# Kernel optimization log

Measured on AMD Instinct MI355X. Metric: run time of the kernel, lower is better.

Reference implementation:

```python
import jax, jax.numpy as jnp
import numpy as np

N, E, D = 50000, 800000, 128
BN_EPS = 1e-5


def mish(x):
    return x * jnp.tanh(jax.nn.softplus(x))


def setup_inputs() -> dict:
    key = jax.random.key(0)
    ks = jax.random.split(key, 16)
    s = 1.0 / np.sqrt(D)
    s2 = 1.0 / np.sqrt(2 * D)
    # unique (row, col) edge pairs so the dense-adjacency edge norm reduces
    # exactly to conv_w[bond_type] + conv_b per edge
    rng = np.random.default_rng(0)
    codes = np.unique(rng.integers(0, N * N, size=2 * E, dtype=np.int64))[:E]
    edge_index = jnp.asarray(np.stack([codes // N, codes % N]), dtype=jnp.int32)
    bond_types = jnp.asarray(rng.integers(0, 4, size=E), dtype=jnp.int32)

    def nrm(k, shape, sc):
        return jax.random.normal(k, shape, jnp.float32) * sc

    return {
        "x": nrm(ks[0], (N, D), 1.0),
        "coords": nrm(ks[1], (N, 3), 1.0),
        "edge_index": edge_index,
        "bond_types": bond_types,
        # NodeFeaturePath
        "W_nb": nrm(ks[2], (2 * D, D), s2), "b_nb": jnp.zeros((D,), jnp.float32),
        "W_nout": nrm(ks[3], (D, D), s), "b_nout": jnp.zeros((D,), jnp.float32),
        # EdgeFeaturePath (1x1 conv over 4 bond-type channels -> scalar per edge)
        "conv_w": nrm(ks[4], (4,), 0.5), "conv_b": jnp.zeros((), jnp.float32),
        "W_el": nrm(ks[5], (2 * D, D), s2), "b_el": jnp.zeros((D,), jnp.float32),
        "W_eout": nrm(ks[6], (D, D), s), "b_eout": jnp.zeros((D,), jnp.float32),
        # StructuralFeaturePath
        "W_coord": nrm(ks[7], (2 * D, D), s2), "b_coord": jnp.zeros((D,), jnp.float32),
        "W_pair": nrm(ks[8], (D, D), s), "b_pair": jnp.zeros((D,), jnp.float32),
        "W_sout": nrm(ks[9], (2 * D, D), s2), "b_sout": jnp.zeros((D,), jnp.float32),
        # FeatureAggregation (att mode, all bias-free)
        "W_init": nrm(ks[10], (D, D), s),
        "feat_lin": nrm(ks[11], (3, D, D), s),
        "W_att": nrm(ks[12], (2 * D, D), s2),
        "W_agg": nrm(ks[13], (D, D), s),
        # BatchNorm (training mode)
        "gamma": jnp.ones((D,), jnp.float32), "beta": jnp.zeros((D,), jnp.float32),
    }


def _forward(x, coords, edge_index, bond_types,
             W_nb, b_nb, W_nout, b_nout,
             conv_w, conv_b, W_el, b_el, W_eout, b_eout,
             W_coord, b_coord, W_pair, b_pair, W_sout, b_sout,
             W_init, feat_lin, W_att, W_agg, gamma, beta):
    act = mish
    src, dst = edge_index[0], edge_index[1]  # PyG: x_j = x[src], x_i = x[dst]
    pair = jnp.concatenate([x[dst], x[src]], axis=1)  # [E, 2D] = [x_i, x_j]

    # --- node path ---
    msg = act(pair @ W_nb + b_nb)                                  # [E, D]
    P = jax.ops.segment_sum(msg, dst, num_segments=N)              # [N, D]
    f_node = act(P @ W_nout + b_nout)

    # --- edge path: 1x1 conv over one-hot bond-type adjacency == lookup ---
    norm_e = (conv_w[bond_types] + conv_b)[:, None]                # [E, 1]
    msg = act((norm_e * pair) @ W_el + b_el)
    P = jax.ops.segment_sum(msg, dst, num_segments=N)
    f_edge = act(P @ W_eout + b_eout)

    # --- struct path ---
    d2 = jnp.sum((coords[src] - coords[dst]) ** 2, axis=1, keepdims=True)  # [E,1]
    msg = (d2 * pair) @ W_coord + b_coord                          # no act in message
    Q = jax.ops.segment_sum(msg, dst, num_segments=N)
    Q = act(Q @ W_pair + b_pair)
    f_struct = act(jnp.concatenate([x, Q], axis=1) @ W_sout + b_sout)

    # --- attention aggregation over the 3 feature paths ---
    feat_stack = jnp.stack([f_node, f_edge, f_struct], axis=0)     # [3, N, D]
    lin_init = act(x @ W_init)[None]                               # [1, N, D] (broadcast of repeat)
    lin_feats = act(jnp.einsum('fnd,fde->fne', feat_stack, feat_lin))
    h = act(jnp.concatenate([jnp.broadcast_to(lin_init, lin_feats.shape), lin_feats], axis=2))
    e = h @ W_att                                                  # [3, N, D]
    a = jax.nn.softmax(e, axis=0)
    att = jnp.sum(a * feat_stack, axis=0)                          # einsum fnd,fnd->nd
    h_agg = att @ W_agg

    # --- batchnorm (training stats, biased var) + final activation ---
    mean = h_agg.mean(axis=0)
    var = h_agg.var(axis=0)
    h_bn = (h_agg - mean) / jnp.sqrt(var + BN_EPS) * gamma + beta
    return act(h_bn)  # final=False


def reference(x, coords, edge_index, bond_types,
              W_nb, b_nb, W_nout, b_nout,
              conv_w, conv_b, W_el, b_el, W_eout, b_eout,
              W_coord, b_coord, W_pair, b_pair, W_sout, b_sout,
              W_init, feat_lin, W_att, W_agg, gamma, beta):
    return _forward(x, coords, edge_index, bond_types,
                    W_nb, b_nb, W_nout, b_nout,
                    conv_w, conv_b, W_el, b_el, W_eout, b_eout,
                    W_coord, b_coord, W_pair, b_pair, W_sout, b_sout,
                    W_init, feat_lin, W_att, W_agg, gamma, beta)
```

## Files before the change

kernel.cpp:

```cpp
#include <hip/hip_runtime.h>
#include <math.h>

#define DD 128
#define LDSS 136
#define PLANE (16 * LDSS)
#define WT 16384

typedef __attribute__((ext_vector_type(8))) short bf16x8;
typedef __attribute__((ext_vector_type(4))) float f32x4;
typedef unsigned short u16;
typedef unsigned int u32;

__device__ __forceinline__ u16 f2bf(float f) {
    u32 u = __builtin_bit_cast(u32, f);
    u += 0x7fffu + ((u >> 16) & 1u);
    return (u16)(u >> 16);
}
__device__ __forceinline__ float bf2f(u16 h) {
    u32 u = ((u32)h) << 16;
    return __builtin_bit_cast(float, u);
}
__device__ __forceinline__ float mishf(float x) {
    float e = __expf(fminf(x, 15.0f));
    float n = e * (e + 2.0f);
    return x * n * __builtin_amdgcn_rcpf(n + 2.0f);
}
__device__ __forceinline__ void splitv(float v, u16& h, u16& l) {
    u32 u = __builtin_bit_cast(u32, v);
    h = (u16)(u >> 16);
    float r = v - __builtin_bit_cast(float, u & 0xffff0000u);
    l = (u16)(__builtin_bit_cast(u32, r) >> 16);
}

__device__ __forceinline__ void zero2(f32x4* acc) {
    f32x4 z4 = {0.f, 0.f, 0.f, 0.f};
    acc[0] = z4; acc[1] = z4;
}

__device__ __forceinline__ void prefetchB4(const u16* __restrict__ Wh, const u16* __restrict__ Wl,
                                           int lane, int ntB, bf16x8* pre)
{
    size_t b0 = (((size_t)ntB + 0) * 64 + lane) * 8;
    size_t b1 = (((size_t)ntB + 1) * 64 + lane) * 8;
    pre[0] = *(const bf16x8*)(Wh + b0);
    pre[1] = *(const bf16x8*)(Wl + b0);
    pre[2] = *(const bf16x8*)(Wh + b1);
    pre[3] = *(const bf16x8*)(Wl + b1);
}

template<int NM, bool SPLIT = false>
__device__ __forceinline__ void gemm2(const bf16x8* ah, const bf16x8* al,
    const u16* __restrict__ Wh, const u16* __restrict__ Wl, int lane, int ntB, f32x4* acc)
{
    f32x4 accB[2];
    if (SPLIT) zero2(accB);
#pragma unroll
    for (int kb = 0; kb < 4; kb++)
#pragma unroll
        for (int j = 0; j < 2; j++) {
            size_t boff = (((size_t)kb * 8 + ntB + j) * 64 + lane) * 8;
            f32x4* ac = (SPLIT && (kb & 1)) ? accB : acc;
            bf16x8 bh = *(const bf16x8*)(Wh + boff);
            ac[j] = __builtin_amdgcn_mfma_f32_16x16x32_bf16(ah[kb], bh, ac[j], 0, 0, 0);
            if (NM >= 2) {
                bf16x8 bl = *(const bf16x8*)(Wl + boff);
                ac[j] = __builtin_amdgcn_mfma_f32_16x16x32_bf16(ah[kb], bl, ac[j], 0, 0, 0);
            }
            if (NM == 3)
                ac[j] = __builtin_amdgcn_mfma_f32_16x16x32_bf16(al[kb], bh, ac[j], 0, 0, 0);
        }
    if (SPLIT) {
        acc[0] += accB[0];
        acc[1] += accB[1];
    }
}

template<int NM, bool SPLIT = false>
__device__ __forceinline__ void gemm2_pre(const bf16x8* ah, const bf16x8* al,
    const u16* __restrict__ Wh, const u16* __restrict__ Wl, int lane, int ntB,
    f32x4* acc, const bf16x8* pre)
{
    f32x4 accB[2];
    if (SPLIT) zero2(accB);
#pragma unroll
    for (int kb = 0; kb < 4; kb++)
#pragma unroll
        for (int j = 0; j < 2; j++) {
            size_t boff = (((size_t)kb * 8 + ntB + j) * 64 + lane) * 8;
            f32x4* ac = (SPLIT && (kb & 1)) ? accB : acc;
            bf16x8 bh = (kb == 0) ? pre[j * 2] : *(const bf16x8*)(Wh + boff);
            ac[j] = __builtin_amdgcn_mfma_f32_16x16x32_bf16(ah[kb], bh, ac[j], 0, 0, 0);
            if (NM >= 2) {
                bf16x8 bl = (kb == 0) ? pre[j * 2 + 1] : *(const bf16x8*)(Wl + boff);
                ac[j] = __builtin_amdgcn_mfma_f32_16x16x32_bf16(ah[kb], bl, ac[j], 0, 0, 0);
            }
            if (NM == 3)
                ac[j] = __builtin_amdgcn_mfma_f32_16x16x32_bf16(al[kb], bh, ac[j], 0, 0, 0);
        }
    if (SPLIT) {
        acc[0] += accB[0];
        acc[1] += accB[1];
    }
}

__device__ __forceinline__ void gemm2_dual_pre(const bf16x8* a1, const bf16x8* a2,
    const u16* __restrict__ W1h, const u16* __restrict__ W1l,
    const u16* __restrict__ W2h, const u16* __restrict__ W2l,
    int lane, int ntB, f32x4* acc1, f32x4* acc2, const bf16x8* pre)
{
#pragma unroll
    for (int kb = 0; kb < 4; kb++)
#pragma unroll
        for (int j = 0; j < 2; j++) {
            size_t boff = (((size_t)kb * 8 + ntB + j) * 64 + lane) * 8;
            bf16x8 b1h = (kb == 0) ? pre[j * 2]     : *(const bf16x8*)(W1h + boff);
            bf16x8 b1l = (kb == 0) ? pre[j * 2 + 1] : *(const bf16x8*)(W1l + boff);
            acc1[j] = __builtin_amdgcn_mfma_f32_16x16x32_bf16(a1[kb], b1h, acc1[j], 0, 0, 0);
            acc1[j] = __builtin_amdgcn_mfma_f32_16x16x32_bf16(a1[kb], b1l, acc1[j], 0, 0, 0);
            bf16x8 b2h = (W2h == W1h) ? b1h : *(const bf16x8*)(W2h + boff);
            bf16x8 b2l = (W2l == W1l) ? b1l : *(const bf16x8*)(W2l + boff);
            acc2[j] = __builtin_amdgcn_mfma_f32_16x16x32_bf16(a2[kb], b2h, acc2[j], 0, 0, 0);
            acc2[j] = __builtin_amdgcn_mfma_f32_16x16x32_bf16(a2[kb], b2l, acc2[j], 0, 0, 0);
        }
}

__device__ __forceinline__ void frag_hi_global16(const u16* __restrict__ src, int row0,
                                                 int lm, int quad, int M, bf16x8* ah)
{
    int row = row0 + lm; if (row >= M) row = M - 1;
    const u16* p = src + (size_t)row * DD + quad * 8;
#pragma unroll
    for (int kb = 0; kb < 4; kb++) ah[kb] = *(const bf16x8*)(p + kb * 32);
}
__device__ __forceinline__ void frag_split_global16(const float* __restrict__ src, int row0,
                                                    int lm, int quad, int M, bf16x8* ah, bf16x8* al)
{
    int row = row0 + lm; if (row >= M) row = M - 1;
    const float* p = src + (size_t)row * DD + quad * 8;
#pragma unroll
    for (int kb = 0; kb < 4; kb++) {
        float tmp[8];
        *(float4*)tmp       = *(const float4*)(p + kb * 32);
        *(float4*)(tmp + 4) = *(const float4*)(p + kb * 32 + 4);
#pragma unroll
        for (int j = 0; j < 8; j++) { u16 h, l; splitv(tmp[j], h, l); ah[kb][j] = (short)h; al[kb][j] = (short)l; }
    }
}
__device__ __forceinline__ void frag_hi_plane16(const u16* P, int lm, int quad, bf16x8* ah)
{
    const u16* p = P + (size_t)lm * LDSS + quad * 8;
#pragma unroll
    for (int kb = 0; kb < 4; kb++) ah[kb] = *(const bf16x8*)(p + kb * 32);
}
__device__ __forceinline__ void frag_planes16(const u16* PH, const u16* PL, int lm, int quad,
                                              bf16x8* ah, bf16x8* al)
{
    const u16* ph = PH + (size_t)lm * LDSS + quad * 8;
    const u16* pl = PL + (size_t)lm * LDSS + quad * 8;
#pragma unroll
    for (int kb = 0; kb < 4; kb++) {
        ah[kb] = *(const bf16x8*)(ph + kb * 32);
        al[kb] = *(const bf16x8*)(pl + kb * 32);
    }
}

struct WSrc { const float* p[18]; };

__global__ __launch_bounds__(256) void prep_weights(WSrc ws, u16* __restrict__ Wh, u16* __restrict__ Wl)
{
    int mat = blockIdx.x >> 3, chunk = blockIdx.x & 7;
    int t = threadIdx.x;
    int tt = chunk * 4 + (t >> 6);
    int lane = t & 63;
    int kb = tt >> 3, nt = tt & 7;
    const float* __restrict__ src = ws.p[mat];
    size_t doff = (size_t)mat * WT + ((size_t)tt * 64 + lane) * 8;
    int srow = kb * 32 + ((lane >> 4) * 8);
    int scol = nt * 16 + (lane & 15);
    u16 th[8], tl[8];
#pragma unroll
    for (int j = 0; j < 8; j++) {
        float v = src[(srow + j) * DD + scol];
        u16 h = f2bf(v);
        th[j] = h;
        tl[j] = f2bf(v - bf2f(h));
    }
    *(bf16x8*)(Wh + doff) = *(bf16x8*)th;
    *(bf16x8*)(Wl + doff) = *(bf16x8*)tl;
}

__global__ __launch_bounds__(256, 4) void fronthist_kernel(
    const float* __restrict__ x, const u16* __restrict__ Wh, const u16* __restrict__ Wl,
    u16* __restrict__ G, u16* __restrict__ xWs,
    float* __restrict__ At, float* __restrict__ Bt, float* __restrict__ Ct,
    const int* __restrict__ ei, int* __restrict__ deg, int E, int M, int NBF)
{
    __shared__ u16 sP[3 * PLANE];
    const int t = threadIdx.x;
    if ((int)blockIdx.x >= NBF) {
        int e = ((int)blockIdx.x - NBF) * 256 + t;
        if (e < E) atomicAdd(&deg[ei[E + e]], 1);
        return;
    }
    u16 *P0 = sP, *P1 = sP + PLANE, *P2 = sP + 2 * PLANE;
    const int wave = t >> 6, lane = t & 63;
    const int lm = lane & 15, quad = lane >> 4;
    const int ntB = wave * 2;
    const int row0 = blockIdx.x * 16;

    bf16x8 ah[4], al[4];
    {
        int row = row0 + lm; if (row >= M) row = M - 1;
        const float* p = x + (size_t)row * DD + quad * 8;
#pragma unroll
        for (int kb = 0; kb < 4; kb++) {
            float tmp[8];
            *(float4*)tmp       = *(const float4*)(p + kb * 32);
            *(float4*)(tmp + 4) = *(const float4*)(p + kb * 32 + 4);
#pragma unroll
            for (int j = 0; j < 8; j++) {
                u16 h, l; splitv(tmp[j], h, l);
                ah[kb][j] = (short)h; al[kb][j] = (short)l;
                if (wave == 0) P0[lm * LDSS + kb * 32 + quad * 8 + j] = f2bf(tmp[j]);
            }
        }
    }
    {
        f32x4 acc[2]; zero2(acc);
        gemm2<1>(ah, ah, Wh + 1 * WT, Wh, lane, ntB, acc);
#pragma unroll
        for (int r = 0; r < 4; r++)
#pragma unroll
            for (int j = 0; j < 2; j++)
                P1[(quad * 4 + r) * LDSS + (ntB + j) * 16 + lm] = f2bf(acc[j][r]);
    }
    {
        f32x4 acc[2]; zero2(acc);
        gemm2<1>(ah, ah, Wh + 3 * WT, Wh, lane, ntB, acc);
#pragma unroll
        for (int r = 0; r < 4; r++)
#pragma unroll
            for (int j = 0; j < 2; j++)
                P2[(quad * 4 + r) * LDSS + (ntB + j) * 16 + lm] = f2bf(acc[j][r]);
    }
    __syncthreads();
#pragma unroll
    for (int i = 0; i < 4; i++) {
        int r = wave * 4 + i;
        int grow = row0 + r;
        if (grow >= M) continue;
        u16* gp = G + (size_t)grow * 384;
        *(u32*)(gp +       lane * 2) = *(const u32*)&P1[r * LDSS + lane * 2];
        *(u32*)(gp + 128 + lane * 2) = *(const u32*)&P2[r * LDSS + lane * 2];
        *(u32*)(gp + 256 + lane * 2) = *(const u32*)&P0[r * LDSS + lane * 2];
    }
    {
        f32x4 acc[2]; zero2(acc);
        gemm2<1>(ah, ah, Wh + 5 * WT, Wh, lane, ntB, acc);
#pragma unroll
        for (int r = 0; r < 4; r++) {
            int grow = row0 + quad * 4 + r;
            if (grow >= M) continue;
#pragma unroll
            for (int j = 0; j < 2; j++)
                xWs[(size_t)grow * DD + (ntB + j) * 16 + lm] = f2bf(acc[j][r]);
        }
    }
    {
        float* outs[3] = {At, Bt, Ct};
        const int mats[3] = {0, 2, 4};
#pragma unroll
        for (int wi = 0; wi < 3; wi++) {
            f32x4 acc[2]; zero2(acc);
            gemm2<3>(ah, al, Wh + (size_t)mats[wi] * WT, Wl + (size_t)mats[wi] * WT, lane, ntB, acc);
            float* out = outs[wi];
#pragma unroll
            for (int r = 0; r < 4; r++) {
                int grow = row0 + quad * 4 + r;
                if (grow >= M) continue;
#pragma unroll
                for (int j = 0; j < 2; j++)
                    out[(size_t)grow * DD + (ntB + j) * 16 + lm] = acc[j][r];
            }
        }
    }
}

__global__ __launch_bounds__(1024) void scan_kernel(const int* __restrict__ deg,
                                                    int* __restrict__ rowptr,
                                                    int* __restrict__ cursor, int N)
{
    __shared__ int sums[1024];
    const int CH = 52;
    int t = threadIdx.x;
    int base = t * CH;
    int local = 0;
#pragma unroll
    for (int i = 0; i < 13; i++) {
        int idx = base + i * 4;
        if (idx + 3 < N) {
            int4 v = *(const int4*)(deg + idx);
            local += v.x + v.y + v.z + v.w;
        } else {
            for (int k = 0; k < 4; k++) if (idx + k < N) local += deg[idx + k];
        }
    }
    sums[t] = local;
    __syncthreads();
    for (int off = 1; off < 1024; off <<= 1) {
        int v = sums[t];
        int u = (t >= off) ? sums[t - off] : 0;
        __syncthreads();
        sums[t] = v + u;
        __syncthreads();
    }
    int run = (t == 0) ? 0 : sums[t - 1];
    for (int i = 0; i < CH; i++) {
        int idx = base + i;
        if (idx < N) {
            rowptr[idx] = run;
            cursor[idx] = run;
            run += deg[idx];
        }
    }
    if (t == 1023) rowptr[N] = sums[1023];
}

__global__ __launch_bounds__(256) void scatter_kernel(
    const int* __restrict__ ei, const int* __restrict__ bond,
    const float* __restrict__ coords, int* __restrict__ cursor,
    int2* __restrict__ csr, int E)
{
    int e = blockIdx.x * 256 + threadIdx.x;
    if (e >= E) return;
    int src = ei[e], dst = ei[E + e];
    int pos = atomicAdd(&cursor[dst], 1);
    float dx = coords[src * 3 + 0] - coords[dst * 3 + 0];
    float dy = coords[src * 3 + 1] - coords[dst * 3 + 1];
    float dz = coords[src * 3 + 2] - coords[dst * 3 + 2];
    float d2 = dx * dx + dy * dy + dz * dz;
    csr[pos] = make_int2(src | (bond[e] << 20), __float_as_int(d2));
}

__global__ __launch_bounds__(256) void edge_agg(
    const float* __restrict__ At, const float* __restrict__ Bt,
    const u16* __restrict__ G,
    const int* __restrict__ rowptr, const int2* __restrict__ csr,
    const float* __restrict__ conv_w, const float* __restrict__ conv_b,
    const float* __restrict__ b_nb, const float* __restrict__ b_el,
    u16* __restrict__ Pn, u16* __restrict__ Pe, float* __restrict__ z,
    float* __restrict__ s_arr, int N)
{
    int wave = threadIdx.x >> 6;
    int lane = threadIdx.x & 63;
    int node = blockIdx.x * 4 + wave;
    if (node >= N) return;
    int c0 = lane * 2;
    float2 at = *(const float2*)(At + (size_t)node * DD + c0);
    float2 bt = *(const float2*)(Bt + (size_t)node * DD + c0);
    float cb = conv_b[0];
    float cw0 = conv_w[0] + cb, cw1 = conv_w[1] + cb, cw2 = conv_w[2] + cb, cw3 = conv_w[3] + cb;
    float bn0 = b_nb[c0], bn1 = b_nb[c0 + 1];
    float be0 = b_el[c0], be1 = b_el[c0 + 1];
    float accn0 = 0.f, accn1 = 0.f, acce0 = 0.f, acce1 = 0.f, accz0 = 0.f, accz1 = 0.f, ssum = 0.f;
    int beg = rowptr[node], end = rowptr[node + 1];

    auto consume = [&](int px, float d2, u32 ga, u32 gb, u32 gx) {
        int bondv = (px >> 20) & 3;
        float w = (bondv == 0) ? cw0 : (bondv == 1) ? cw1 : (bondv == 2) ? cw2 : cw3;
        float a0 = __builtin_bit_cast(float, ga << 16), a1 = __builtin_bit_cast(float, ga & 0xffff0000u);
        float b0 = __builtin_bit_cast(float, gb << 16), b1 = __builtin_bit_cast(float, gb & 0xffff0000u);
        float x0 = __builtin_bit_cast(float, gx << 16), x1 = __builtin_bit_cast(float, gx & 0xffff0000u);
        accn0 += mishf(at.x + a0 + bn0);
        accn1 += mishf(at.y + a1 + bn1);
        acce0 += mishf(w * (bt.x + b0) + be0);
        acce1 += mishf(w * (bt.y + b1) + be1);
        accz0 += d2 * x0;
        accz1 += d2 * x1;
        ssum += d2;
    };

    int k = beg;
    for (; k + 4 <= end; k += 4) {
        int2 pd0 = csr[k], pd1 = csr[k + 1], pd2 = csr[k + 2], pd3 = csr[k + 3];
        const u16* g0 = G + (size_t)(pd0.x & 0xFFFFF) * 384;
        const u16* g1 = G + (size_t)(pd1.x & 0xFFFFF) * 384;
        const u16* g2 = G + (size_t)(pd2.x & 0xFFFFF) * 384;
        const u16* g3 = G + (size_t)(pd3.x & 0xFFFFF) * 384;
        u32 ga0 = *(const u32*)(g0 + c0), gb0 = *(const u32*)(g0 + 128 + c0), gx0 = *(const u32*)(g0 + 256 + c0);
        u32 ga1 = *(const u32*)(g1 + c0), gb1 = *(const u32*)(g1 + 128 + c0), gx1 = *(const u32*)(g1 + 256 + c0);
        u32 ga2 = *(const u32*)(g2 + c0), gb2 = *(const u32*)(g2 + 128 + c0), gx2 = *(const u32*)(g2 + 256 + c0);
        u32 ga3 = *(const u32*)(g3 + c0), gb3 = *(const u32*)(g3 + 128 + c0), gx3 = *(const u32*)(g3 + 256 + c0);
        consume(pd0.x, __int_as_float(pd0.y), ga0, gb0, gx0);
        consume(pd1.x, __int_as_float(pd1.y), ga1, gb1, gx1);
        consume(pd2.x, __int_as_float(pd2.y), ga2, gb2, gx2);
        consume(pd3.x, __int_as_float(pd3.y), ga3, gb3, gx3);
    }
    for (; k < end; k++) {
        int2 pd = csr[k];
        const u16* gp = G + (size_t)(pd.x & 0xFFFFF) * 384;
        u32 ga = *(const u32*)(gp + c0);
        u32 gb = *(const u32*)(gp + 128 + c0);
        u32 gx = *(const u32*)(gp + 256 + c0);
        consume(pd.x, __int_as_float(pd.y), ga, gb, gx);
    }

    *(u32*)(Pn + (size_t)node * DD + c0) = (u32)f2bf(accn0) | ((u32)f2bf(accn1) << 16);
    *(u32*)(Pe + (size_t)node * DD + c0) = (u32)f2bf(acce0) | ((u32)f2bf(acce1) << 16);
    *(float2*)(z + (size_t)node * DD + c0) = make_float2(accz0, accz1);
    if (lane == 0) s_arr[node] = ssum;
}

__global__ __launch_bounds__(256, 3) void mega_kernel(
    const u16* __restrict__ Pn, const u16* __restrict__ Pe, const float* __restrict__ z,
    const float* __restrict__ Ct, const u16* __restrict__ xWs,
    const float* __restrict__ s_arr, const int* __restrict__ deg,
    const float* __restrict__ b_nout, const float* __restrict__ b_eout,
    const float* __restrict__ b_coord, const float* __restrict__ b_pair,
    const float* __restrict__ b_sout,
    const u16* __restrict__ Wh, const u16* __restrict__ Wl,
    float* __restrict__ hout, float* __restrict__ bnsums, int M)
{
    __shared__ u16 sP[4 * PLANE];
    u16 *PA = sP, *PB = sP + PLANE, *PC = sP + 2 * PLANE, *PD = sP + 3 * PLANE;
    const int t = threadIdx.x, wave = t >> 6, lane = t & 63;
    const int lm = lane & 15, quad = lane >> 4;
    const int ntB = wave * 2;
    const int row0 = blockIdx.x * 16;

    u32 f1p[4], f2p[4], f3p[4];
    float d1v[8], d2v[8];
    bf16x8 preB[4];

    {
        bf16x8 an[4], ae[4];
        f32x4 accn[2], acce[2];
        prefetchB4(Wh + 11 * WT, Wl + 11 * WT, lane, ntB, preB);
        frag_hi_global16(Pn, row0, lm, quad, M, an);
        frag_hi_global16(Pe, row0, lm, quad, M, ae);
        zero2(accn); zero2(acce);
        gemm2_dual_pre(an, ae, Wh + 11 * WT, Wl + 11 * WT, Wh + 12 * WT, Wl + 12 * WT, lane, ntB, accn, acce, preB);
#pragma unroll
        for (int r = 0; r < 4; r++) {
            u32 pkn = 0, pke = 0;
#pragma unroll
            for (int j = 0; j < 2; j++) {
                int col = (ntB + j) * 16 + lm;
                int lidx = (quad * 4 + r) * LDSS + col;
                u16 hn = f2bf(mishf(accn[j][r] + b_nout[col]));
                u16 he = f2bf(mishf(acce[j][r] + b_eout[col]));
                pkn |= ((u32)hn) << (16 * j);
                pke |= ((u32)he) << (16 * j);
                PA[lidx] = hn; PB[lidx] = he;
            }
            f1p[r] = pkn; f2p[r] = pke;
        }
        prefetchB4(Wh + 13 * WT, Wl + 13 * WT, lane, ntB, preB);
        __syncthreads();
        frag_hi_plane16(PA, lm, quad, an);
        frag_hi_plane16(PB, lm, quad, ae);
        zero2(accn); zero2(acce);
        gemm2_dual_pre(an, ae, Wh + 13 * WT, Wl + 13 * WT, Wh + 14 * WT, Wl + 14 * WT, lane, ntB, accn, acce, preB);
#pragma unroll
        for (int r = 0; r < 4; r++)
#pragma unroll
            for (int j = 0; j < 2; j++) {
                int lidx = (quad * 4 + r) * LDSS + (ntB + j) * 16 + lm;
                PC[lidx] = f2bf(mishf(mishf(accn[j][r])));
                PD[lidx] = f2bf(mishf(mishf(acce[j][r])));
            }
        prefetchB4(Wh + 16 * WT, Wl + 16 * WT, lane, ntB, preB);
        __syncthreads();
        frag_hi_plane16(PC, lm, quad, an);
        frag_hi_plane16(PD, lm, quad, ae);
        zero2(accn); zero2(acce);
        gemm2_dual_pre(an, ae, Wh + 16 * WT, Wl + 16 * WT, Wh + 16 * WT, Wl + 16 * WT, lane, ntB, accn, acce, preB);
#pragma unroll
        for (int r = 0; r < 4; r++)
#pragma unroll
            for (int j = 0; j < 2; j++) {
                d1v[r * 2 + j] = accn[j][r];
                d2v[r * 2 + j] = acce[j][r];
            }
    }

    bf16x8 ah[4], al[4];
    f32x4 acc[2];
    prefetchB4(Wh + 8 * WT, Wl + 8 * WT, lane, ntB, preB);
    frag_split_global16(z, row0, lm, quad, M, ah, al);
    zero2(acc);
    gemm2_pre<3, true>(ah, al, Wh + 8 * WT, Wl + 8 * WT, lane, ntB, acc, preB);
#pragma unroll
    for (int r = 0; r < 4; r++) {
        int crow = row0 + quad * 4 + r; if (crow >= M) crow = M - 1;
        float sv = s_arr[crow];
        float dv = (float)deg[crow];
#pragma unroll
        for (int j = 0; j < 2; j++) {
            int col = (ntB + j) * 16 + lm;
            float v = acc[j][r] + sv * Ct[(size_t)crow * DD + col] + dv * b_coord[col];
            int lidx = (quad * 4 + r) * LDSS + col;
            u16 h, l; splitv(v, h, l); PA[lidx] = h; PB[lidx] = l;
        }
    }
    prefetchB4(Wh + 9 * WT, Wl + 9 * WT, lane, ntB, preB);
    __syncthreads();
    frag_planes16(PA, PB, lm, quad, ah, al);
    zero2(acc);
    gemm2_pre<3, true>(ah, al, Wh + 9 * WT, Wl + 9 * WT, lane, ntB, acc, preB);
#pragma unroll
    for (int r = 0; r < 4; r++)
#pragma unroll
        for (int j = 0; j < 2; j++) {
            int col = (ntB + j) * 16 + lm;
            int lidx = (quad * 4 + r) * LDSS + col;
            u16 h, l; splitv(mishf(acc[j][r] + b_pair[col]), h, l); PC[lidx] = h; PD[lidx] = l;
        }
    prefetchB4(Wh + 10 * WT, Wl + 10 * WT, lane, ntB, preB);
    __syncthreads();
    frag_planes16(PC, PD, lm, quad, ah, al);
    zero2(acc);
    gemm2_pre<3, true>(ah, al, Wh + 10 * WT, Wl + 10 * WT, lane, ntB, acc, preB);
#pragma unroll
    for (int r = 0; r < 4; r++) {
        int crow = row0 + quad * 4 + r; if (crow >= M) crow = M - 1;
        u32 pk = 0;
#pragma unroll
        for (int j = 0; j < 2; j++) {
            int col = (ntB + j) * 16 + lm;
            float v = mishf(acc[j][r] + bf2f(xWs[(size_t)crow * DD + col]) + b_sout[col]);
            u16 h, l; splitv(v, h, l);
            pk |= ((u32)f2bf(v)) << (16 * j);
            int lidx = (quad * 4 + r) * LDSS + col;
            PA[lidx] = h; PB[lidx] = l;
        }
        f3p[r] = pk;
    }
    prefetchB4(Wh + 15 * WT, Wl + 15 * WT, lane, ntB, preB);
    __syncthreads();
    frag_planes16(PA, PB, lm, quad, ah, al);
    zero2(acc);
    gemm2_pre<3, true>(ah, al, Wh + 15 * WT, Wl + 15 * WT, lane, ntB, acc, preB);
#pragma unroll
    for (int r = 0; r < 4; r++)
#pragma unroll
        for (int j = 0; j < 2; j++) {
            int lidx = (quad * 4 + r) * LDSS + (ntB + j) * 16 + lm;
            u16 h, l; splitv(mishf(mishf(acc[j][r])), h, l); PC[lidx] = h; PD[lidx] = l;
        }
    prefetchB4(Wh + 16 * WT, Wl + 16 * WT, lane, ntB, preB);
    __syncthreads();
    frag_planes16(PC, PD, lm, quad, ah, al);
    zero2(acc);
    gemm2_pre<3, true>(ah, al, Wh + 16 * WT, Wl + 16 * WT, lane, ntB, acc, preB);

#pragma unroll
    for (int r = 0; r < 4; r++)
#pragma unroll
        for (int j = 0; j < 2; j++) {
            int i = r * 2 + j;
            float x1 = d1v[i], x2 = d2v[i], x3 = acc[j][r];
            float m = fmaxf(fmaxf(x1, x2), x3);
            float p1 = __expf(x1 - m), p2 = __expf(x2 - m), p3 = __expf(x3 - m);
            float fv1 = bf2f((u16)(f1p[r] >> (16 * j)));
            float fv2 = bf2f((u16)(f2p[r] >> (16 * j)));
            float fv3 = bf2f((u16)(f3p[r] >> (16 * j)));
            float att = (p1 * fv1 + p2 * fv2 + p3 * fv3) * __builtin_amdgcn_rcpf(p1 + p2 + p3);
            int lidx = (quad * 4 + r) * LDSS + (ntB + j) * 16 + lm;
            u16 h, l; splitv(att, h, l); PA[lidx] = h; PB[lidx] = l;
        }
    prefetchB4(Wh + 17 * WT, Wl + 17 * WT, lane, ntB, preB);
    __syncthreads();
    frag_planes16(PA, PB, lm, quad, ah, al);
    zero2(acc);
    gemm2_pre<3, true>(ah, al, Wh + 17 * WT, Wl + 17 * WT, lane, ntB, acc, preB);
    float s[2] = {0.f, 0.f}, q[2] = {0.f, 0.f};
#pragma unroll
    for (int r = 0; r < 4; r++) {
        int grow = row0 + quad * 4 + r;
        if (grow >= M) continue;
#pragma unroll
        for (int j = 0; j < 2; j++) {
            float v = acc[j][r];
            hout[(size_t)grow * DD + (ntB + j) * 16 + lm] = v;
            s[j] += v; q[j] += v * v;
        }
    }
    __syncthreads();
    float* red = (float*)sP;
    if (t < 128) { red[t] = 0.f; red[128 + t] = 0.f; }
    __syncthreads();
#pragma unroll
    for (int j = 0; j < 2; j++) {
        int col = (ntB + j) * 16 + lm;
        atomicAdd(&red[col], s[j]);
        atomicAdd(&red[128 + col], q[j]);
    }
    __syncthreads();
    if (t < 128) {
        atomicAdd(&bnsums[t], red[t]);
        atomicAdd(&bnsums[128 + t], red[128 + t]);
    }
}

__global__ void bn_finalize(const float* __restrict__ sums, const float* __restrict__ gamma,
                            const float* __restrict__ beta, float* __restrict__ scale,
                            float* __restrict__ shift, float n_inv)
{
    int c = threadIdx.x;
    float mean = sums[c] * n_inv;
    float var = sums[128 + c] * n_inv - mean * mean;
    float inv = rsqrtf(var + 1e-5f);
    float sc = gamma[c] * inv;
    scale[c] = sc;
    shift[c] = beta[c] - mean * sc;
}

__global__ __launch_bounds__(256) void bn_apply(float* __restrict__ h, const float* __restrict__ scale,
                                                const float* __restrict__ shift, size_t total4)
{
    size_t idx = (size_t)blockIdx.x * 256 + threadIdx.x;
    if (idx >= total4) return;
    size_t off = idx * 4;
    int c = (int)(off & 127);
    float4 v = *(const float4*)(h + off);
    float4 sc = *(const float4*)(scale + c);
    float4 sh = *(const float4*)(shift + c);
    v.x = mishf(v.x * sc.x + sh.x);
    v.y = mishf(v.y * sc.y + sh.y);
    v.z = mishf(v.z * sc.z + sh.z);
    v.w = mishf(v.w * sc.w + sh.w);
    *(float4*)(h + off) = v;
}

extern "C" void kernel_launch(void* const* d_in, const int* in_sizes, int n_in,
                              void* d_out, int out_size, void* d_ws, size_t ws_size,
                              hipStream_t stream)
{
    (void)n_in; (void)out_size; (void)ws_size;
    const float* x       = (const float*)d_in[0];
    const float* coords  = (const float*)d_in[1];
    const int*   ei      = (const int*)d_in[2];
    const int*   bond    = (const int*)d_in[3];
    const float* W_nb    = (const float*)d_in[4];
    const float* b_nb    = (const float*)d_in[5];
    const float* W_nout  = (const float*)d_in[6];
    const float* b_nout  = (const float*)d_in[7];
    const float* conv_w  = (const float*)d_in[8];
    const float* conv_b  = (const float*)d_in[9];
    const float* W_el    = (const float*)d_in[10];
    const float* b_el    = (const float*)d_in[11];
    const float* W_eout  = (const float*)d_in[12];
    const float* b_eout  = (const float*)d_in[13];
    const float* W_coord = (const float*)d_in[14];
    const float* b_coord = (const float*)d_in[15];
    const float* W_pair  = (const float*)d_in[16];
    const float* b_pair  = (const float*)d_in[17];
    const float* W_sout  = (const float*)d_in[18];
    const float* b_sout  = (const float*)d_in[19];
    const float* W_init  = (const float*)d_in[20];
    const float* feat_lin= (const float*)d_in[21];
    const float* W_att   = (const float*)d_in[22];
    const float* W_agg   = (const float*)d_in[23];
    const float* gamma   = (const float*)d_in[24];
    const float* beta    = (const float*)d_in[25];

    const int N = in_sizes[0] / DD;
    const int E = in_sizes[3];
    const size_t ND = (size_t)N * DD;
    const int SUB = DD * DD;
    const int NB16 = (N + 15) / 16;
    const int EB   = (E + 255) / 256;

    char* base = (char*)d_ws;
    size_t off = 0;
    auto alloc = [&](size_t bytes) -> char* {
        char* p = base + off;
        off = (off + bytes + 63) & ~(size_t)63;
        return p;
    };
    u16*   G    = (u16*)alloc((size_t)N * 384 * 2);
    u16*   xWs  = (u16*)alloc(ND * 2);
    float* At   = (float*)alloc(ND * 4);
    float* Bt   = (float*)alloc(ND * 4);
    float* Ct   = (float*)alloc(ND * 4);
    u16*   Pn   = (u16*)alloc(ND * 2);
    u16*   Pe   = (u16*)alloc(ND * 2);
    float* z    = (float*)alloc(ND * 4);
    u16*   Wh   = (u16*)alloc((size_t)18 * WT * 2);
    u16*   Wl   = (u16*)alloc((size_t)18 * WT * 2);
    int2*  csr  = (int2*)alloc((size_t)E * 8);
    int*   deg    = (int*)alloc((size_t)(N + 64) * 4);
    int*   rowptr = (int*)alloc((size_t)(N + 1) * 4);
    int*   cursor = (int*)alloc((size_t)N * 4);
    float* s_arr  = (float*)alloc((size_t)N * 4);
    float* bnsums  = (float*)alloc(256 * 4);
    float* bnscale = (float*)alloc(128 * 4);
    float* bnshift = (float*)alloc(128 * 4);

    float* hout = (float*)d_out;

    WSrc wsrc;
    wsrc.p[0] = W_nb;            wsrc.p[1] = W_nb + SUB;
    wsrc.p[2] = W_el;            wsrc.p[3] = W_el + SUB;
    wsrc.p[4] = W_coord;         wsrc.p[5] = W_sout;
    wsrc.p[6] = W_init;          wsrc.p[7] = W_att;
    wsrc.p[8] = W_coord + SUB;   wsrc.p[9] = W_pair;
    wsrc.p[10] = W_sout + SUB;   wsrc.p[11] = W_nout;
    wsrc.p[12] = W_eout;         wsrc.p[13] = feat_lin;
    wsrc.p[14] = feat_lin + SUB; wsrc.p[15] = feat_lin + 2 * SUB;
    wsrc.p[16] = W_att + SUB;    wsrc.p[17] = W_agg;

    const dim3 blk256(256);
    const size_t total4 = ND / 4;
    const dim3 gElem((unsigned)((total4 + 255) / 256));

    hipMemsetAsync(deg, 0, (size_t)N * 4, stream);
    hipMemsetAsync(bnsums, 0, 256 * 4, stream);

    prep_weights<<<dim3(18 * 8), blk256, 0, stream>>>(wsrc, Wh, Wl);
    fronthist_kernel<<<dim3(NB16 + EB), blk256, 0, stream>>>(x, Wh, Wl, G, xWs, At, Bt, Ct,
                                                             ei, deg, E, N, NB16);
    scan_kernel<<<1, 1024, 0, stream>>>(deg, rowptr, cursor, N);
    scatter_kernel<<<dim3(EB), blk256, 0, stream>>>(ei, bond, coords, cursor, csr, E);

    edge_agg<<<(N + 3) / 4, blk256, 0, stream>>>(At, Bt, G, rowptr, csr, conv_w, conv_b,
                                                 b_nb, b_el, Pn, Pe, z, s_arr, N);

    mega_kernel<<<NB16, blk256, 0, stream>>>(Pn, Pe, z, Ct, xWs, s_arr, deg,
                                             b_nout, b_eout, b_coord, b_pair, b_sout,
                                             Wh, Wl, hout, bnsums, N);

    bn_finalize<<<1, 128, 0, stream>>>(bnsums, gamma, beta, bnscale, bnshift, 1.0f / (float)N);
    bn_apply<<<gElem, blk256, 0, stream>>>(hout, bnscale, bnshift, total4);
}
```

Measured before the change: 599.2 us.

## Interleave gathered node table per lane, deepen edge gather batching and weight prefetch

```diff
diff --git a/kernel.cpp b/kernel.cpp
--- a/kernel.cpp
+++ b/kernel.cpp
@@ -10,6 +10,7 @@
 typedef __attribute__((ext_vector_type(4))) float f32x4;
 typedef unsigned short u16;
 typedef unsigned int u32;
+struct u32x3 { u32 x, y, z; };
 
 __device__ __forceinline__ u16 f2bf(float f) {
     u32 u = __builtin_bit_cast(u32, f);
@@ -37,15 +38,17 @@
     acc[0] = z4; acc[1] = z4;
 }
 
-__device__ __forceinline__ void prefetchB4(const u16* __restrict__ Wh, const u16* __restrict__ Wl,
+__device__ __forceinline__ void prefetchB8(const u16* __restrict__ Wh, const u16* __restrict__ Wl,
                                            int lane, int ntB, bf16x8* pre)
 {
-    size_t b0 = (((size_t)ntB + 0) * 64 + lane) * 8;
-    size_t b1 = (((size_t)ntB + 1) * 64 + lane) * 8;
-    pre[0] = *(const bf16x8*)(Wh + b0);
-    pre[1] = *(const bf16x8*)(Wl + b0);
-    pre[2] = *(const bf16x8*)(Wh + b1);
-    pre[3] = *(const bf16x8*)(Wl + b1);
+#pragma unroll
+    for (int kb = 0; kb < 2; kb++)
+#pragma unroll
+        for (int j = 0; j < 2; j++) {
+            size_t b = (((size_t)kb * 8 + ntB + j) * 64 + lane) * 8;
+            pre[(kb * 2 + j) * 2]     = *(const bf16x8*)(Wh + b);
+            pre[(kb * 2 + j) * 2 + 1] = *(const bf16x8*)(Wl + b);
+        }
 }
 
 template<int NM, bool SPLIT = false>
@@ -88,10 +91,10 @@
         for (int j = 0; j < 2; j++) {
             size_t boff = (((size_t)kb * 8 + ntB + j) * 64 + lane) * 8;
             f32x4* ac = (SPLIT && (kb & 1)) ? accB : acc;
-            bf16x8 bh = (kb == 0) ? pre[j * 2] : *(const bf16x8*)(Wh + boff);
+            bf16x8 bh = (kb < 2) ? pre[(kb * 2 + j) * 2] : *(const bf16x8*)(Wh + boff);
             ac[j] = __builtin_amdgcn_mfma_f32_16x16x32_bf16(ah[kb], bh, ac[j], 0, 0, 0);
             if (NM >= 2) {
-                bf16x8 bl = (kb == 0) ? pre[j * 2 + 1] : *(const bf16x8*)(Wl + boff);
+                bf16x8 bl = (kb < 2) ? pre[(kb * 2 + j) * 2 + 1] : *(const bf16x8*)(Wl + boff);
                 ac[j] = __builtin_amdgcn_mfma_f32_16x16x32_bf16(ah[kb], bl, ac[j], 0, 0, 0);
             }
             if (NM == 3)
@@ -113,8 +116,8 @@
 #pragma unroll
         for (int j = 0; j < 2; j++) {
             size_t boff = (((size_t)kb * 8 + ntB + j) * 64 + lane) * 8;
-            bf16x8 b1h = (kb == 0) ? pre[j * 2]     : *(const bf16x8*)(W1h + boff);
-            bf16x8 b1l = (kb == 0) ? pre[j * 2 + 1] : *(const bf16x8*)(W1l + boff);
+            bf16x8 b1h = (kb < 2) ? pre[(kb * 2 + j) * 2]     : *(const bf16x8*)(W1h + boff);
+            bf16x8 b1l = (kb < 2) ? pre[(kb * 2 + j) * 2 + 1] : *(const bf16x8*)(W1l + boff);
             acc1[j] = __builtin_amdgcn_mfma_f32_16x16x32_bf16(a1[kb], b1h, acc1[j], 0, 0, 0);
             acc1[j] = __builtin_amdgcn_mfma_f32_16x16x32_bf16(a1[kb], b1l, acc1[j], 0, 0, 0);
             bf16x8 b2h = (W2h == W1h) ? b1h : *(const bf16x8*)(W2h + boff);
@@ -249,10 +252,12 @@
         int r = wave * 4 + i;
         int grow = row0 + r;
         if (grow >= M) continue;
-        u16* gp = G + (size_t)grow * 384;
-        *(u32*)(gp +       lane * 2) = *(const u32*)&P1[r * LDSS + lane * 2];
-        *(u32*)(gp + 128 + lane * 2) = *(const u32*)&P2[r * LDSS + lane * 2];
-        *(u32*)(gp + 256 + lane * 2) = *(const u32*)&P0[r * LDSS + lane * 2];
+        u16* gp = G + (size_t)grow * 384 + lane * 6;
+        u32x3 v;
+        v.x = *(const u32*)&P1[r * LDSS + lane * 2];
+        v.y = *(const u32*)&P2[r * LDSS + lane * 2];
+        v.z = *(const u32*)&P0[r * LDSS + lane * 2];
+        *(u32x3*)gp = v;
     }
     {
         f32x4 acc[2]; zero2(acc);
@@ -356,6 +361,7 @@
     int node = blockIdx.x * 4 + wave;
     if (node >= N) return;
     int c0 = lane * 2;
+    int lane6 = lane * 6;
     float2 at = *(const float2*)(At + (size_t)node * DD + c0);
     float2 bt = *(const float2*)(Bt + (size_t)node * DD + c0);
     float cb = conv_b[0];
@@ -381,28 +387,34 @@
     };
 
     int k = beg;
+    for (; k + 8 <= end; k += 8) {
+        int2 pd[8];
+        u32x3 g[8];
+#pragma unroll
+        for (int i = 0; i < 8; i++) pd[i] = csr[k + i];
+#pragma unroll
+        for (int i = 0; i < 8; i++)
+            g[i] = *(const u32x3*)(G + (size_t)(pd[i].x & 0xFFFFF) * 384 + lane6);
+#pragma unroll
+        for (int i = 0; i < 8; i++)
+            consume(pd[i].x, __int_as_float(pd[i].y), g[i].x, g[i].y, g[i].z);
+    }
     for (; k + 4 <= end; k += 4) {
-        int2 pd0 = csr[k], pd1 = csr[k + 1], pd2 = csr[k + 2], pd3 = csr[k + 3];
-        const u16* g0 = G + (size_t)(pd0.x & 0xFFFFF) * 384;
-        const u16* g1 = G + (size_t)(pd1.x & 0xFFFFF) * 384;
-        const u16* g2 = G + (size_t)(pd2.x & 0xFFFFF) * 384;
-        const u16* g3 = G + (size_t)(pd3.x & 0xFFFFF) * 384;
-        u32 ga0 = *(const u32*)(g0 + c0), gb0 = *(const u32*)(g0 + 128 + c0), gx0 = *(const u32*)(g0 + 256 + c0);
-        u32 ga1 = *(const u32*)(g1 + c0), gb1 = *(const u32*)(g1 + 128 + c0), gx1 = *(const u32*)(g1 + 256 + c0);
-        u32 ga2 = *(const u32*)(g2 + c0), gb2 = *(const u32*)(g2 + 128 + c0), gx2 = *(const u32*)(g2 + 256 + c0);
-        u32 ga3 = *(const u32*)(g3 + c0), gb3 = *(const u32*)(g3 + 128 + c0), gx3 = *(const u32*)(g3 + 256 + c0);
-        consume(pd0.x, __int_as_float(pd0.y), ga0, gb0, gx0);
-        consume(pd1.x, __int_as_float(pd1.y), ga1, gb1, gx1);
-        consume(pd2.x, __int_as_float(pd2.y), ga2, gb2, gx2);
-        consume(pd3.x, __int_as_float(pd3.y), ga3, gb3, gx3);
+        int2 pd[4];
+        u32x3 g[4];
+#pragma unroll
+        for (int i = 0; i < 4; i++) pd[i] = csr[k + i];
+#pragma unroll
+        for (int i = 0; i < 4; i++)
+            g[i] = *(const u32x3*)(G + (size_t)(pd[i].x & 0xFFFFF) * 384 + lane6);
+#pragma unroll
+        for (int i = 0; i < 4; i++)
+            consume(pd[i].x, __int_as_float(pd[i].y), g[i].x, g[i].y, g[i].z);
     }
     for (; k < end; k++) {
         int2 pd = csr[k];
-        const u16* gp = G + (size_t)(pd.x & 0xFFFFF) * 384;
-        u32 ga = *(const u32*)(gp + c0);
-        u32 gb = *(const u32*)(gp + 128 + c0);
-        u32 gx = *(const u32*)(gp + 256 + c0);
-        consume(pd.x, __int_as_float(pd.y), ga, gb, gx);
+        u32x3 g = *(const u32x3*)(G + (size_t)(pd.x & 0xFFFFF) * 384 + lane6);
+        consume(pd.x, __int_as_float(pd.y), g.x, g.y, g.z);
     }
 
     *(u32*)(Pn + (size_t)node * DD + c0) = (u32)f2bf(accn0) | ((u32)f2bf(accn1) << 16);
@@ -430,12 +442,12 @@
 
     u32 f1p[4], f2p[4], f3p[4];
     float d1v[8], d2v[8];
-    bf16x8 preB[4];
+    bf16x8 preB[8];
 
     {
         bf16x8 an[4], ae[4];
         f32x4 accn[2], acce[2];
-        prefetchB4(Wh + 11 * WT, Wl + 11 * WT, lane, ntB, preB);
+        prefetchB8(Wh + 11 * WT, Wl + 11 * WT, lane, ntB, preB);
         frag_hi_global16(Pn, row0, lm, quad, M, an);
         frag_hi_global16(Pe, row0, lm, quad, M, ae);
         zero2(accn); zero2(acce);
@@ -455,7 +467,7 @@
             }
             f1p[r] = pkn; f2p[r] = pke;
         }
-        prefetchB4(Wh + 13 * WT, Wl + 13 * WT, lane, ntB, preB);
+        prefetchB8(Wh + 13 * WT, Wl + 13 * WT, lane, ntB, preB);
         __syncthreads();
         frag_hi_plane16(PA, lm, quad, an);
         frag_hi_plane16(PB, lm, quad, ae);
@@ -469,7 +481,7 @@
                 PC[lidx] = f2bf(mishf(mishf(accn[j][r])));
                 PD[lidx] = f2bf(mishf(mishf(acce[j][r])));
             }
-        prefetchB4(Wh + 16 * WT, Wl + 16 * WT, lane, ntB, preB);
+        prefetchB8(Wh + 16 * WT, Wl + 16 * WT, lane, ntB, preB);
         __syncthreads();
         frag_hi_plane16(PC, lm, quad, an);
         frag_hi_plane16(PD, lm, quad, ae);
@@ -486,7 +498,7 @@
 
     bf16x8 ah[4], al[4];
     f32x4 acc[2];
-    prefetchB4(Wh + 8 * WT, Wl + 8 * WT, lane, ntB, preB);
+    prefetchB8(Wh + 8 * WT, Wl + 8 * WT, lane, ntB, preB);
     frag_split_global16(z, row0, lm, quad, M, ah, al);
     zero2(acc);
     gemm2_pre<3, true>(ah, al, Wh + 8 * WT, Wl + 8 * WT, lane, ntB, acc, preB);
@@ -503,7 +515,7 @@
             u16 h, l; splitv(v, h, l); PA[lidx] = h; PB[lidx] = l;
         }
     }
-    prefetchB4(Wh + 9 * WT, Wl + 9 * WT, lane, ntB, preB);
+    prefetchB8(Wh + 9 * WT, Wl + 9 * WT, lane, ntB, preB);
     __syncthreads();
     frag_planes16(PA, PB, lm, quad, ah, al);
     zero2(acc);
@@ -516,7 +528,7 @@
             int lidx = (quad * 4 + r) * LDSS + col;
             u16 h, l; splitv(mishf(acc[j][r] + b_pair[col]), h, l); PC[lidx] = h; PD[lidx] = l;
         }
-    prefetchB4(Wh + 10 * WT, Wl + 10 * WT, lane, ntB, preB);
+    prefetchB8(Wh + 10 * WT, Wl + 10 * WT, lane, ntB, preB);
     __syncthreads();
     frag_planes16(PC, PD, lm, quad, ah, al);
     zero2(acc);
@@ -536,7 +548,7 @@
         }
         f3p[r] = pk;
     }
-    prefetchB4(Wh + 15 * WT, Wl + 15 * WT, lane, ntB, preB);
+    prefetchB8(Wh + 15 * WT, Wl + 15 * WT, lane, ntB, preB);
     __syncthreads();
     frag_planes16(PA, PB, lm, quad, ah, al);
     zero2(acc);
@@ -548,7 +560,7 @@
             int lidx = (quad * 4 + r) * LDSS + (ntB + j) * 16 + lm;
             u16 h, l; splitv(mishf(mishf(acc[j][r])), h, l); PC[lidx] = h; PD[lidx] = l;
         }
-    prefetchB4(Wh + 16 * WT, Wl + 16 * WT, lane, ntB, preB);
+    prefetchB8(Wh + 16 * WT, Wl + 16 * WT, lane, ntB, preB);
     __syncthreads();
     frag_planes16(PC, PD, lm, quad, ah, al);
     zero2(acc);
@@ -569,7 +581,7 @@
             int lidx = (quad * 4 + r) * LDSS + (ntB + j) * 16 + lm;
             u16 h, l; splitv(att, h, l); PA[lidx] = h; PB[lidx] = l;
         }
-    prefetchB4(Wh + 17 * WT, Wl + 17 * WT, lane, ntB, preB);
+    prefetchB8(Wh + 17 * WT, Wl + 17 * WT, lane, ntB, preB);
     __syncthreads();
     frag_planes16(PA, PB, lm, quad, ah, al);
     zero2(acc);
```

Result: no change. 594.6 us (-0.8%).
